# Performance work log

Measured on AMD Instinct MI355X. Metric: run time of the kernel, lower is better.

The kernel has to match this reference:

```python
import jax, jax.numpy as jnp
import numpy as np

D_MODEL, D_K, D_V, H, B = 1024, 64, 64, 16, 32768


def _xavier(key, fan_in, fan_out):
    std = float(np.sqrt(2.0 / (fan_in + fan_out)))
    return jax.random.normal(key, (fan_in, fan_out), dtype=jnp.float32) * std


def setup_inputs() -> dict:
    key = jax.random.key(0)
    ks = jax.random.split(key, 7)
    return {
        "queries": jax.random.normal(ks[0], (B, D_MODEL), dtype=jnp.float32),
        "keys": jax.random.normal(ks[1], (B, D_MODEL), dtype=jnp.float32),
        "values": jax.random.normal(ks[2], (B, D_MODEL), dtype=jnp.float32),
        "Wq": _xavier(ks[3], D_MODEL, H * D_K),
        "bq": jnp.zeros((H * D_K,), jnp.float32),
        "Wk": _xavier(ks[4], D_MODEL, H * D_K),
        "bk": jnp.zeros((H * D_K,), jnp.float32),
        "Wv": _xavier(ks[5], D_MODEL, H * D_V),
        "bv": jnp.zeros((H * D_V,), jnp.float32),
        "Wo": _xavier(ks[6], H * D_V, D_MODEL),
        "bo": jnp.zeros((D_MODEL,), jnp.float32),
    }


def reference(queries, keys, values, Wq, bq, Wk, bk, Wv, bv, Wo, bo):
    b = queries.shape[0]
    q = (queries @ Wq + bq).reshape(b, H, D_K)   # (b, h, d_k)
    k = (keys @ Wk + bk).reshape(b, H, D_K)      # (b, h, d_k)
    v = (values @ Wv + bv).reshape(b, H, D_V)    # (b, h, d_v)
    # attention over heads: (b, h, h)
    att = jnp.einsum('bhd,bgd->bhg', q, k) / jnp.sqrt(jnp.float32(D_K))
    att = jax.nn.softmax(att, axis=-1)
    out = jnp.einsum('bhg,bgd->bhd', att, v).reshape(b, H * D_V)
    return out @ Wo + bo
```

## Files before the change

### kernel.cpp

```cpp
#include <hip/hip_runtime.h>

typedef __attribute__((ext_vector_type(8))) unsigned short u16x8;
typedef __attribute__((ext_vector_type(8))) short s16x8;
typedef __attribute__((ext_vector_type(4))) float f32x4;

#define D_MODEL 1024
#define NROWS 32768
#define BK 64
#define NT 16

__device__ __forceinline__ unsigned short f2bf(float f) {
  union { float f; unsigned int u; } c; c.f = f;
  return (unsigned short)((c.u + 0x7fffu + ((c.u >> 16) & 1u)) >> 16);
}
__device__ __forceinline__ float bf2f(unsigned short h) {
  union { unsigned int u; float f; } c; c.u = ((unsigned int)h) << 16;
  return c.f;
}
__device__ __forceinline__ unsigned int cvtpk_bf16(float lo, float hi) {
  unsigned int r;
  asm("v_cvt_pk_bf16_f32 %0, %1, %2" : "=v"(r) : "v"(lo), "v"(hi));
  return r;
}

__device__ __forceinline__ void gload_lds16(const void* gsrc, void* ldst) {
  const __attribute__((address_space(1))) void* g =
      reinterpret_cast<const __attribute__((address_space(1))) void*>(
          reinterpret_cast<unsigned long long>(gsrc));
  __attribute__((address_space(3))) void* l =
      reinterpret_cast<__attribute__((address_space(3))) void*>(
          static_cast<unsigned int>(reinterpret_cast<unsigned long long>(ldst)));
  __builtin_amdgcn_global_load_lds(g, l, 16, 0, 0);
}

#define BAR() asm volatile("s_barrier" ::: "memory")

__global__ __launch_bounds__(256) void wtrans_kernel(
    const float* __restrict__ W0, const float* __restrict__ W1,
    const float* __restrict__ W2, const float* __restrict__ W3,
    unsigned short* __restrict__ T0, unsigned short* __restrict__ T1,
    unsigned short* __restrict__ T2, unsigned short* __restrict__ T3) {
  const float* W = blockIdx.z == 0 ? W0 : blockIdx.z == 1 ? W1 : blockIdx.z == 2 ? W2 : W3;
  unsigned short* T = blockIdx.z == 0 ? T0 : blockIdx.z == 1 ? T1 : blockIdx.z == 2 ? T2 : T3;
  __shared__ float tile[32][33];
  const int tx = threadIdx.x & 31, ty = threadIdx.x >> 5;
  const int n0 = blockIdx.x * 32, k0 = blockIdx.y * 32;
#pragma unroll
  for (int i = 0; i < 4; ++i)
    tile[ty + 8 * i][tx] = W[(size_t)(k0 + ty + 8 * i) * D_MODEL + n0 + tx];
  __syncthreads();
#pragma unroll
  for (int i = 0; i < 4; ++i)
    T[(size_t)(n0 + ty + 8 * i) * D_MODEL + k0 + tx] = f2bf(tile[tx][ty + 8 * i]);
}

#define MFMA16(p, A00, A01, A10, A11)                                                        \
  _Pragma("unroll") for (int n = 0; n < 4; ++n) {                                            \
    acc[2*(p)][n]   = __builtin_amdgcn_mfma_f32_16x16x32_bf16(A00, bfr[n][0], acc[2*(p)][n], 0, 0, 0);   \
    acc[2*(p)][n]   = __builtin_amdgcn_mfma_f32_16x16x32_bf16(A01, bfr[n][1], acc[2*(p)][n], 0, 0, 0);   \
    acc[2*(p)+1][n] = __builtin_amdgcn_mfma_f32_16x16x32_bf16(A10, bfr[n][0], acc[2*(p)+1][n], 0, 0, 0); \
    acc[2*(p)+1][n] = __builtin_amdgcn_mfma_f32_16x16x32_bf16(A11, bfr[n][1], acc[2*(p)+1][n], 0, 0, 0); \
  }

#define LDA_(Ac, m, ksoff) (*(const s16x8*)((Ac) + (wm * 128 + (m) * 16 + lrow) * 128 + (ksoff)))
#define LDB_(Bc, n, ksoff) (*(const s16x8*)((Bc) + (wn * 64 + (n) * 16 + lrow) * 128 + (ksoff)))

template <bool A_FP32, bool OUT_BF16>
__device__ __forceinline__ void gemm8p_body(
    const void* __restrict__ Ap, const unsigned short* __restrict__ BT,
    const float* __restrict__ bias, void* __restrict__ Cp, char* smem) {
  const int tid = threadIdx.x;
  const int lane = tid & 63, wid = tid >> 6;
  const int wm = wid >> 2, wn = wid & 3;
  const int lrow = lane & 15, lkg = lane >> 4;

  const int id = blockIdx.y * gridDim.x + blockIdx.x;
  const int sw = (id & 7) * 64 + (id >> 3);
  const int mbase = (sw >> 2) * 256;
  const int nbase = (sw & 3) * 256;

  char* const Ab0 = smem;
  char* const Ab1 = smem + 32768;
  char* const Bb0 = smem + 65536;
  char* const Bb1 = smem + 98304;

  const int sgoff = (((tid & 7) ^ ((tid >> 3) & 7)) * 8);
  const int srow = tid >> 3;
  const int soff0 = ((0 + lkg) ^ (lrow & 7)) * 16;
  const int soff1 = ((4 + lkg) ^ (lrow & 7)) * 16;
  const int ldsw = wid * 1024;

  auto stA = [&](int u, int half) {
    const unsigned short* G =
        (const unsigned short*)Ap + (size_t)(mbase + half * 128 + srow) * D_MODEL + u * BK + sgoff;
    char* L = ((u & 1) ? Ab1 : Ab0) + half * 16384 + ldsw;
    gload_lds16(G, L);
    gload_lds16(G + (size_t)64 * D_MODEL, L + 8192);
  };
  auto stB = [&](int u, int half) {
    const unsigned short* G =
        BT + (size_t)(nbase + half * 128 + srow) * D_MODEL + u * BK + sgoff;
    char* L = ((u & 1) ? Bb1 : Bb0) + half * 16384 + ldsw;
    gload_lds16(G, L);
    gload_lds16(G + (size_t)64 * D_MODEL, L + 8192);
  };

  f32x4 fa[8];
  auto ldA = [&](int u, int half) {
    const float* G = (const float*)Ap +
        (size_t)(mbase + half * 128 + srow) * D_MODEL + u * BK + (tid & 7) * 8;
    fa[half * 4 + 0] = *(const f32x4*)G;
    fa[half * 4 + 1] = *(const f32x4*)(G + 4);
    fa[half * 4 + 2] = *(const f32x4*)(G + (size_t)64 * D_MODEL);
    fa[half * 4 + 3] = *(const f32x4*)(G + (size_t)64 * D_MODEL + 4);
  };
  auto wrA = [&](int u) {
    char* Abuf = ((u & 1) ? Ab1 : Ab0);
#pragma unroll
    for (int h = 0; h < 2; ++h) {
#pragma unroll
      for (int rr = 0; rr < 2; ++rr) {
        f32x4 lo = fa[h * 4 + rr * 2 + 0];
        f32x4 hi = fa[h * 4 + rr * 2 + 1];
        union { unsigned int w[4]; u16x8 v; } pk;
        pk.w[0] = cvtpk_bf16(lo[0], lo[1]);
        pk.w[1] = cvtpk_bf16(lo[2], lo[3]);
        pk.w[2] = cvtpk_bf16(hi[0], hi[1]);
        pk.w[3] = cvtpk_bf16(hi[2], hi[3]);
        const int r = srow + rr * 64;
        *(u16x8*)(Abuf + h * 16384 + r * 128 + (((tid & 7) ^ (r & 7)) * 16)) = pk.v;
      }
    }
    asm volatile("s_waitcnt lgkmcnt(0)" ::: "memory");
  };

  f32x4 acc[8][4];
  f32x4 zero = {0.f, 0.f, 0.f, 0.f};
#pragma unroll
  for (int m = 0; m < 8; ++m)
#pragma unroll
    for (int n = 0; n < 4; ++n) acc[m][n] = zero;
  s16x8 bfr[4][2];

  if constexpr (A_FP32) {
    ldA(0, 0); ldA(0, 1);
    stB(0, 0); stB(0, 1);
    stB(1, 0); stB(1, 1);
    asm volatile("s_waitcnt vmcnt(8)" ::: "memory");
    wrA(0);
    asm volatile("s_waitcnt vmcnt(4)" ::: "memory");
  } else {
    stA(0, 0); stA(0, 1); stB(0, 0); stB(0, 1);
    stB(1, 0); stB(1, 1);
    asm volatile("s_waitcnt vmcnt(4)" ::: "memory");
  }
  BAR();

#pragma unroll 1
  for (int u = 0; u < NT; ++u) {
    char* Ac = (u & 1) ? Ab1 : Ab0;
    char* Bc = (u & 1) ? Bb1 : Bb0;
    {
      s16x8 a00 = LDA_(Ac, 0, soff0), a01 = LDA_(Ac, 0, soff1);
      s16x8 a10 = LDA_(Ac, 1, soff0), a11 = LDA_(Ac, 1, soff1);
#pragma unroll
      for (int n = 0; n < 4; ++n) { bfr[n][0] = LDB_(Bc, n, soff0); bfr[n][1] = LDB_(Bc, n, soff1); }
      if (u + 1 < NT) { if constexpr (A_FP32) ldA(u + 1, 0); else stA(u + 1, 0); }
      BAR();
      __builtin_amdgcn_s_setprio(1);
      MFMA16(0, a00, a01, a10, a11);
      __builtin_amdgcn_s_setprio(0);
      BAR();
    }
    {
      s16x8 a00 = LDA_(Ac, 2, soff0), a01 = LDA_(Ac, 2, soff1);
      s16x8 a10 = LDA_(Ac, 3, soff0), a11 = LDA_(Ac, 3, soff1);
      if (u + 1 < NT) { if constexpr (A_FP32) ldA(u + 1, 1); else stA(u + 1, 1); }
      BAR();
      __builtin_amdgcn_s_setprio(1);
      MFMA16(1, a00, a01, a10, a11);
      __builtin_amdgcn_s_setprio(0);
      BAR();
    }
    {
      s16x8 a00 = LDA_(Ac, 4, soff0), a01 = LDA_(Ac, 4, soff1);
      s16x8 a10 = LDA_(Ac, 5, soff0), a11 = LDA_(Ac, 5, soff1);
      if constexpr (A_FP32) {
        asm volatile("s_waitcnt vmcnt(0)" ::: "memory");
        if (u + 1 < NT) wrA(u + 1);
      }
      if (u + 2 < NT) stB(u + 2, 0);
      BAR();
      __builtin_amdgcn_s_setprio(1);
      MFMA16(2, a00, a01, a10, a11);
      __builtin_amdgcn_s_setprio(0);
      BAR();
    }
    {
      s16x8 a00 = LDA_(Ac, 6, soff0), a01 = LDA_(Ac, 6, soff1);
      s16x8 a10 = LDA_(Ac, 7, soff0), a11 = LDA_(Ac, 7, soff1);
      if (u + 2 < NT) stB(u + 2, 1);
      if constexpr (!A_FP32) {
        if (u + 2 < NT) {
          asm volatile("s_waitcnt vmcnt(4)" ::: "memory");
        } else {
          asm volatile("s_waitcnt vmcnt(0)" ::: "memory");
        }
      }
      BAR();
      __builtin_amdgcn_s_setprio(1);
      MFMA16(3, a00, a01, a10, a11);
      __builtin_amdgcn_s_setprio(0);
      BAR();
    }
  }

  const size_t crow0 = mbase + wm * 128;
  const int ccol0 = nbase + wn * 64;
#pragma unroll
  for (int m = 0; m < 8; ++m) {
#pragma unroll
    for (int n = 0; n < 4; ++n) {
      const int col = ccol0 + n * 16 + lrow;
      const float bv = bias[col];
#pragma unroll
      for (int r = 0; r < 4; ++r) {
        const size_t row = crow0 + m * 16 + lkg * 4 + r;
        const float v = acc[m][n][r] + bv;
        if constexpr (OUT_BF16)
          ((unsigned short*)Cp)[row * D_MODEL + col] = f2bf(v);
        else
          ((float*)Cp)[row * D_MODEL + col] = v;
      }
    }
  }
}

__global__ __launch_bounds__(512, 1) void qkv_gemm8(
    const float* __restrict__ Xq, const float* __restrict__ Xk, const float* __restrict__ Xv,
    const unsigned short* __restrict__ WqT, const unsigned short* __restrict__ WkT,
    const unsigned short* __restrict__ WvT,
    const float* __restrict__ bq, const float* __restrict__ bk, const float* __restrict__ bv,
    unsigned short* __restrict__ Qb, unsigned short* __restrict__ Kb,
    unsigned short* __restrict__ Vb) {
  extern __shared__ char smem[];
  const int z = blockIdx.z;
  gemm8p_body<true, true>(z == 0 ? (const void*)Xq : z == 1 ? (const void*)Xk : (const void*)Xv,
                          z == 0 ? WqT : z == 1 ? WkT : WvT,
                          z == 0 ? bq : z == 1 ? bk : bv,
                          z == 0 ? (void*)Qb : z == 1 ? (void*)Kb : (void*)Vb, smem);
}

__global__ __launch_bounds__(512, 1) void out_gemm8(
    const unsigned short* __restrict__ Ob, const unsigned short* __restrict__ WoT,
    const float* __restrict__ bo, float* __restrict__ out) {
  extern __shared__ char smem[];
  gemm8p_body<false, false>(Ob, WoT, bo, out, smem);
}

__global__ __launch_bounds__(256) void attn_kernel(
    const unsigned short* __restrict__ Qb, const unsigned short* __restrict__ Kb,
    const unsigned short* __restrict__ Vb, unsigned short* __restrict__ Ob) {
  __shared__ __align__(16) unsigned short sm[4][3][16 * 72];
  const int tid = threadIdx.x, lane = tid & 63, wid = tid >> 6;
  const size_t row = (size_t)blockIdx.x * 4 + wid;
  const unsigned short* srcs[3] = {Qb + row * 1024, Kb + row * 1024, Vb + row * 1024};
#pragma unroll
  for (int m = 0; m < 3; ++m) {
#pragma unroll
    for (int i = 0; i < 2; ++i) {
      int c = lane * 2 + i;
      int h = c >> 3, col = (c & 7) * 8;
      *(u16x8*)&sm[wid][m][h * 72 + col] = *(const u16x8*)(srcs[m] + h * 64 + col);
    }
  }
  __syncthreads();

  const int h = lane & 15, gq = lane >> 4;
  float s[4] = {0.f, 0.f, 0.f, 0.f};
#pragma unroll
  for (int dc = 0; dc < 8; ++dc) {
    u16x8 qv = *(const u16x8*)&sm[wid][0][h * 72 + dc * 8];
    float qf[8];
#pragma unroll
    for (int e = 0; e < 8; ++e) qf[e] = bf2f(qv[e]);
#pragma unroll
    for (int j = 0; j < 4; ++j) {
      u16x8 kv = *(const u16x8*)&sm[wid][1][(gq * 4 + j) * 72 + dc * 8];
#pragma unroll
      for (int e = 0; e < 8; ++e) s[j] += qf[e] * bf2f(kv[e]);
    }
  }
  float mx = s[0];
#pragma unroll
  for (int j = 0; j < 4; ++j) { s[j] *= 0.125f; mx = fmaxf(mx * (j == 0 ? 0.125f : 1.f), s[j]); }
  mx = fmaxf(mx, __shfl_xor(mx, 16, 64));
  mx = fmaxf(mx, __shfl_xor(mx, 32, 64));
  float p[4], sum = 0.f;
#pragma unroll
  for (int j = 0; j < 4; ++j) { p[j] = __expf(s[j] - mx); sum += p[j]; }
  sum += __shfl_xor(sum, 16, 64);
  sum += __shfl_xor(sum, 32, 64);
  const float rinv = 1.0f / sum;
  float pall[16];
#pragma unroll
  for (int t = 0; t < 4; ++t)
#pragma unroll
    for (int j = 0; j < 4; ++j) pall[t * 4 + j] = __shfl(p[j], h + 16 * t, 64);
  float o[16];
#pragma unroll
  for (int e = 0; e < 16; ++e) o[e] = 0.f;
  const int db = gq * 16;
#pragma unroll
  for (int g = 0; g < 16; ++g) {
    float pg = pall[g];
    u16x8 v0 = *(const u16x8*)&sm[wid][2][g * 72 + db];
    u16x8 v1 = *(const u16x8*)&sm[wid][2][g * 72 + db + 8];
#pragma unroll
    for (int e = 0; e < 8; ++e) { o[e] += pg * bf2f(v0[e]); o[8 + e] += pg * bf2f(v1[e]); }
  }
  u16x8 r0, r1;
#pragma unroll
  for (int e = 0; e < 8; ++e) { r0[e] = f2bf(o[e] * rinv); r1[e] = f2bf(o[8 + e] * rinv); }
  unsigned short* dst = Ob + row * 1024 + h * 64 + db;
  *(u16x8*)dst = r0;
  *(u16x8*)(dst + 8) = r1;
}

extern "C" void kernel_launch(void* const* d_in, const int* in_sizes, int n_in,
                              void* d_out, int out_size, void* d_ws, size_t ws_size,
                              hipStream_t stream) {
  const float* queries = (const float*)d_in[0];
  const float* keys    = (const float*)d_in[1];
  const float* values  = (const float*)d_in[2];
  const float* Wq = (const float*)d_in[3];
  const float* bq = (const float*)d_in[4];
  const float* Wk = (const float*)d_in[5];
  const float* bk = (const float*)d_in[6];
  const float* Wv = (const float*)d_in[7];
  const float* bv = (const float*)d_in[8];
  const float* Wo = (const float*)d_in[9];
  const float* bo = (const float*)d_in[10];
  float* out = (float*)d_out;

  unsigned short* ws = (unsigned short*)d_ws;
  const size_t WE = (size_t)1024 * 1024;
  const size_t XE = (size_t)NROWS * 1024;
  unsigned short* WqT = ws;
  unsigned short* WkT = WqT + WE;
  unsigned short* WvT = WkT + WE;
  unsigned short* WoT = WvT + WE;
  unsigned short* Qb  = WoT + WE;
  unsigned short* Kb  = Qb + XE;
  unsigned short* Vb  = Kb + XE;
  unsigned short* Ob  = Vb + XE;

  hipFuncSetAttribute((const void*)qkv_gemm8, hipFuncAttributeMaxDynamicSharedMemorySize, 131072);
  hipFuncSetAttribute((const void*)out_gemm8, hipFuncAttributeMaxDynamicSharedMemorySize, 131072);

  wtrans_kernel<<<dim3(32, 32, 4), 256, 0, stream>>>(Wq, Wk, Wv, Wo, WqT, WkT, WvT, WoT);
  qkv_gemm8<<<dim3(4, 128, 3), 512, 131072, stream>>>(
      queries, keys, values, WqT, WkT, WvT, bq, bk, bv, Qb, Kb, Vb);
  attn_kernel<<<dim3(NROWS / 4), 256, 0, stream>>>(Qb, Kb, Vb, Ob);
  out_gemm8<<<dim3(4, 128, 1), 512, 131072, stream>>>(Ob, WoT, bo, out);
}
```

Measured before the change: 445.1 us.

## Prefetch fp32 A tiles two steps ahead and split LDS write per half

For the fp32-A GEMM path, global loads of A are issued two k-tiles ahead instead of one. The bf16 conversion and LDS write are split into two halves placed in different sub-phases, each followed by an lgkmcnt wait. This removes the full vmcnt(0) stall before the A write in the third sub-phase, so global load latency can hide behind more MFMA work. The cost is more in-flight registers (fa holds the next tile while it is written) and tighter vmcnt accounting, which could be wrong if the counts don't match the issued loads.

```diff
diff --git a/kernel.cpp b/kernel.cpp
--- a/kernel.cpp
+++ b/kernel.cpp
@@ -114,24 +114,20 @@
     fa[half * 4 + 2] = *(const f32x4*)(G + (size_t)64 * D_MODEL);
     fa[half * 4 + 3] = *(const f32x4*)(G + (size_t)64 * D_MODEL + 4);
   };
-  auto wrA = [&](int u) {
-    char* Abuf = ((u & 1) ? Ab1 : Ab0);
-#pragma unroll
-    for (int h = 0; h < 2; ++h) {
-#pragma unroll
-      for (int rr = 0; rr < 2; ++rr) {
-        f32x4 lo = fa[h * 4 + rr * 2 + 0];
-        f32x4 hi = fa[h * 4 + rr * 2 + 1];
-        union { unsigned int w[4]; u16x8 v; } pk;
-        pk.w[0] = cvtpk_bf16(lo[0], lo[1]);
-        pk.w[1] = cvtpk_bf16(lo[2], lo[3]);
-        pk.w[2] = cvtpk_bf16(hi[0], hi[1]);
-        pk.w[3] = cvtpk_bf16(hi[2], hi[3]);
-        const int r = srow + rr * 64;
-        *(u16x8*)(Abuf + h * 16384 + r * 128 + (((tid & 7) ^ (r & 7)) * 16)) = pk.v;
-      }
-    }
-    asm volatile("s_waitcnt lgkmcnt(0)" ::: "memory");
+  auto wrA_half = [&](int u, int half) {
+    char* Abuf = ((u & 1) ? Ab1 : Ab0) + half * 16384;
+#pragma unroll
+    for (int rr = 0; rr < 2; ++rr) {
+      f32x4 lo = fa[half * 4 + rr * 2 + 0];
+      f32x4 hi = fa[half * 4 + rr * 2 + 1];
+      union { unsigned int w[4]; u16x8 v; } pk;
+      pk.w[0] = cvtpk_bf16(lo[0], lo[1]);
+      pk.w[1] = cvtpk_bf16(lo[2], lo[3]);
+      pk.w[2] = cvtpk_bf16(hi[0], hi[1]);
+      pk.w[3] = cvtpk_bf16(hi[2], hi[3]);
+      const int r = srow + rr * 64;
+      *(u16x8*)(Abuf + r * 128 + (((tid & 7) ^ (r & 7)) * 16)) = pk.v;
+    }
   };
 
   f32x4 acc[8][4];
@@ -145,10 +141,11 @@
   if constexpr (A_FP32) {
     ldA(0, 0); ldA(0, 1);
     stB(0, 0); stB(0, 1);
+    wrA_half(0, 0); wrA_half(0, 1);
+    ldA(1, 0); ldA(1, 1);
     stB(1, 0); stB(1, 1);
-    asm volatile("s_waitcnt vmcnt(8)" ::: "memory");
-    wrA(0);
-    asm volatile("s_waitcnt vmcnt(4)" ::: "memory");
+    asm volatile("s_waitcnt vmcnt(12)" ::: "memory");
+    asm volatile("s_waitcnt lgkmcnt(0)" ::: "memory");
   } else {
     stA(0, 0); stA(0, 1); stB(0, 0); stB(0, 1);
     stB(1, 0); stB(1, 1);
@@ -165,7 +162,7 @@
       s16x8 a10 = LDA_(Ac, 1, soff0), a11 = LDA_(Ac, 1, soff1);
 #pragma unroll
       for (int n = 0; n < 4; ++n) { bfr[n][0] = LDB_(Bc, n, soff0); bfr[n][1] = LDB_(Bc, n, soff1); }
-      if (u + 1 < NT) { if constexpr (A_FP32) ldA(u + 1, 0); else stA(u + 1, 0); }
+      if constexpr (!A_FP32) { if (u + 1 < NT) stA(u + 1, 0); }
       BAR();
       __builtin_amdgcn_s_setprio(1);
       MFMA16(0, a00, a01, a10, a11);
@@ -175,7 +172,7 @@
     {
       s16x8 a00 = LDA_(Ac, 2, soff0), a01 = LDA_(Ac, 2, soff1);
       s16x8 a10 = LDA_(Ac, 3, soff0), a11 = LDA_(Ac, 3, soff1);
-      if (u + 1 < NT) { if constexpr (A_FP32) ldA(u + 1, 1); else stA(u + 1, 1); }
+      if constexpr (!A_FP32) { if (u + 1 < NT) stA(u + 1, 1); }
       BAR();
       __builtin_amdgcn_s_setprio(1);
       MFMA16(1, a00, a01, a10, a11);
@@ -186,10 +183,11 @@
       s16x8 a00 = LDA_(Ac, 4, soff0), a01 = LDA_(Ac, 4, soff1);
       s16x8 a10 = LDA_(Ac, 5, soff0), a11 = LDA_(Ac, 5, soff1);
       if constexpr (A_FP32) {
-        asm volatile("s_waitcnt vmcnt(0)" ::: "memory");
-        if (u + 1 < NT) wrA(u + 1);
+        if (u + 1 < NT) wrA_half(u + 1, 0);
+        if (u + 2 < NT) ldA(u + 2, 0);
       }
       if (u + 2 < NT) stB(u + 2, 0);
+      if constexpr (A_FP32) asm volatile("s_waitcnt lgkmcnt(0)" ::: "memory");
       BAR();
       __builtin_amdgcn_s_setprio(1);
       MFMA16(2, a00, a01, a10, a11);
@@ -199,14 +197,20 @@
     {
       s16x8 a00 = LDA_(Ac, 6, soff0), a01 = LDA_(Ac, 6, soff1);
       s16x8 a10 = LDA_(Ac, 7, soff0), a11 = LDA_(Ac, 7, soff1);
+      if constexpr (A_FP32) {
+        if (u + 1 < NT) wrA_half(u + 1, 1);
+        if (u + 2 < NT) ldA(u + 2, 1);
+      }
       if (u + 2 < NT) stB(u + 2, 1);
-      if constexpr (!A_FP32) {
-        if (u + 2 < NT) {
+      if (u + 2 < NT) {
+        if constexpr (A_FP32)
+          asm volatile("s_waitcnt vmcnt(12)" ::: "memory");
+        else
           asm volatile("s_waitcnt vmcnt(4)" ::: "memory");
-        } else {
-          asm volatile("s_waitcnt vmcnt(0)" ::: "memory");
-        }
+      } else {
+        asm volatile("s_waitcnt vmcnt(0)" ::: "memory");
       }
+      if constexpr (A_FP32) asm volatile("s_waitcnt lgkmcnt(0)" ::: "memory");
       BAR();
       __builtin_amdgcn_s_setprio(1);
       MFMA16(3, a00, a01, a10, a11);
```

Result: slower. 481.5 us (+8.2%).
